# Performance work log

Hardware: AMD Instinct MI355X
Metric: run time of the kernel (lower is better)

## Reference

```python
import jax, jax.numpy as jnp
import numpy as np

N_NODES = 50000
N_EDGES = 800000
IN_CH = 128
HID = 128


def setup_inputs() -> dict:
    key = jax.random.key(0)
    ks = jax.random.split(key, 16)
    inp = {
        "x": jax.random.normal(ks[0], (N_NODES, IN_CH), dtype=jnp.float32),
        "edge_index": jax.random.randint(ks[1], (2, N_EDGES), 0, N_NODES, dtype=jnp.int64),
        "batch_size": 1024,
    }
    dims = [(IN_CH, HID), (HID, HID), (HID, HID)]
    for i, (din, dout) in enumerate(dims):
        s = 1.0 / np.sqrt(din)
        inp[f"W_l{i}"] = jax.random.uniform(ks[2 + 4 * i], (dout, din), jnp.float32, -s, s)
        inp[f"b_l{i}"] = jax.random.uniform(ks[3 + 4 * i], (dout,), jnp.float32, -s, s)
        inp[f"W_r{i}"] = jax.random.uniform(ks[4 + 4 * i], (dout, din), jnp.float32, -s, s)
        inp[f"a{i}"] = jnp.full((dout,), 0.25, dtype=jnp.float32)  # PReLU slope
    return inp


def _sage_prelu(x, src, dst, W_l, b_l, W_r, a):
    # mean aggregation of source messages at target nodes
    msg_sum = jax.ops.segment_sum(x[src], dst, num_segments=N_NODES)  # [N, din]
    deg = jax.ops.segment_sum(jnp.ones((src.shape[0],), x.dtype), dst, num_segments=N_NODES)
    agg = msg_sum / jnp.maximum(deg, 1.0)[:, None]
    out = agg @ W_l.T + b_l + x @ W_r.T  # lin_l(aggr) + lin_r(x), bias on lin_l only
    return jnp.where(out > 0, out, a * out)  # per-channel PReLU


def reference(x, edge_index, batch_size, W_l0, b_l0, W_r0, a0, W_l1, b_l1, W_r1, a1, W_l2, b_l2, W_r2, a2):
    src, dst = edge_index[0], edge_index[1]
    x = _sage_prelu(x, src, dst, W_l0, b_l0, W_r0, a0)
    x = _sage_prelu(x, src, dst, W_l1, b_l1, W_r1, a1)
    x = _sage_prelu(x, src, dst, W_l2, b_l2, W_r2, a2)
    return x[:batch_size]
```

## Files before the change

### kernel.cpp

```cpp
#include <hip/hip_runtime.h>

#define NN 50000
#define NE 800000
#define C 128
#define CAP 64
#define EP4 ((NE / 4 + 255) / 256)
#define SPLITB 1563
#define WB 96
#define CB  ((NN + 255) / 256)
#define AGG0B ((NN + 3) / 4)
#define ASTRIDE 136

typedef __attribute__((ext_vector_type(8))) short bf16x8;
typedef __attribute__((ext_vector_type(4))) float f32x4;
typedef unsigned short ushort;

__device__ inline ushort bf16_rn(float f) {
    unsigned u = __builtin_bit_cast(unsigned, f);
    u += 0x7FFF + ((u >> 16) & 1);
    return (ushort)(u >> 16);
}
__device__ inline void split_bf16(float f, ushort& hi, ushort& lo) {
    hi = bf16_rn(f);
    float hif = __builtin_bit_cast(float, (unsigned)hi << 16);
    lo = bf16_rn(f - hif);
}
__device__ inline float bf_lo(unsigned u) { return __builtin_bit_cast(float, u << 16); }
__device__ inline float bf_hi(unsigned u) { return __builtin_bit_cast(float, u & 0xFFFF0000u); }


__global__ __launch_bounds__(256)
void prep_kernel(const int* __restrict__ src, const int* __restrict__ dst,
                 const float* __restrict__ x,
                 const float* __restrict__ W0, const float* __restrict__ W1,
                 const float* __restrict__ W2, const float* __restrict__ W3,
                 const float* __restrict__ W4, const float* __restrict__ W5,
                 int* __restrict__ deg, int* __restrict__ col,
                 ushort* __restrict__ Ah, ushort* __restrict__ Al,
                 ushort* __restrict__ Wh, ushort* __restrict__ Wl,
                 int* __restrict__ needed, int rows_out) {
    int t = threadIdx.x;
    if (blockIdx.x < EP4) {
        int e0 = (blockIdx.x * 256 + t) * 4;
        if (e0 < NE) {
            int4 da = *(const int4*)(dst + e0);
            int4 sa = *(const int4*)(src + e0);
            int p0 = atomicAdd(&deg[da.x], 1);
            int p1 = atomicAdd(&deg[da.y], 1);
            int p2 = atomicAdd(&deg[da.z], 1);
            int p3 = atomicAdd(&deg[da.w], 1);
            if (p0 < CAP) col[da.x * CAP + p0] = sa.x;
            if (p1 < CAP) col[da.y * CAP + p1] = sa.y;
            if (p2 < CAP) col[da.z * CAP + p2] = sa.z;
            if (p3 < CAP) col[da.w * CAP + p3] = sa.w;
            if (da.x < rows_out) needed[sa.x] = 1;
            if (da.y < rows_out) needed[sa.y] = 1;
            if (da.z < rows_out) needed[sa.z] = 1;
            if (da.w < rows_out) needed[sa.w] = 1;
        }
    } else if (blockIdx.x < EP4 + SPLITB) {
        int tid = (blockIdx.x - EP4) * 256 + t;
        const int total = NN * C / 4;
        for (int i = tid; i < total; i += SPLITB * 256) {
            f32x4 v = ((const f32x4*)x)[i];
            ushort h0, h1, h2, h3, l0, l1, l2, l3;
            split_bf16(v.x, h0, l0);
            split_bf16(v.y, h1, l1);
            split_bf16(v.z, h2, l2);
            split_bf16(v.w, h3, l3);
            *(uint2*)(Ah + (size_t)i * 4) = make_uint2((unsigned)h0 | ((unsigned)h1 << 16),
                                                       (unsigned)h2 | ((unsigned)h3 << 16));
            *(uint2*)(Al + (size_t)i * 4) = make_uint2((unsigned)l0 | ((unsigned)l1 << 16),
                                                       (unsigned)l2 | ((unsigned)l3 << 16));
        }
    } else {
        const float* Ws[6] = {W0, W1, W2, W3, W4, W5};
        int i = (blockIdx.x - EP4 - SPLITB) * 256 + t;
        int mat = i >> 12;
        f32x4 v = ((const f32x4*)Ws[mat])[i & 4095];
        ushort h0, h1, h2, h3, l0, l1, l2, l3;
        split_bf16(v.x, h0, l0);
        split_bf16(v.y, h1, l1);
        split_bf16(v.z, h2, l2);
        split_bf16(v.w, h3, l3);
        *(uint2*)(Wh + (size_t)i * 4) = make_uint2((unsigned)h0 | ((unsigned)h1 << 16),
                                                   (unsigned)h2 | ((unsigned)h3 << 16));
        *(uint2*)(Wl + (size_t)i * 4) = make_uint2((unsigned)l0 | ((unsigned)l1 << 16),
                                                   (unsigned)l2 | ((unsigned)l3 << 16));
    }
}


__global__ __launch_bounds__(256)
void agg_kernel(const ushort* __restrict__ xh, const int* __restrict__ deg,
                const int* __restrict__ col,
                const int* __restrict__ list, const int* __restrict__ countp,
                ushort* __restrict__ aggh, ushort* __restrict__ aggl, int nodes,
                int aggblocks, const int* __restrict__ needed,
                int* __restrict__ wlist, int* __restrict__ wcnt, int rows_out) {
    if (needed && blockIdx.x >= aggblocks) {
        int i = (blockIdx.x - aggblocks) * 256 + threadIdx.x;
        if (i < NN && (i < rows_out || needed[i])) {
            int p = atomicAdd(wcnt, 1);
            wlist[p] = i;
        }
        return;
    }
    int i = (blockIdx.x * blockDim.x + threadIdx.x) >> 6;
    int lane = threadIdx.x & 63;
    int cnt = list ? *countp : nodes;
    if (i >= cnt) return;
    int node = list ? list[i] : i;
    int quad = lane >> 4;
    int ql   = lane & 15;
    int d = min(deg[node], CAP);
    int start = node * CAP;
    int end = start + d;
    const uint4* xr = (const uint4*)xh;
    float a0=0,a1=0,a2=0,a3=0,a4=0,a5=0,a6=0,a7=0;
    int e = start;
    for (; e + 7 < end; e += 8) {
        int i0 = col[e + quad];
        int i1 = col[e + 4 + quad];
        uint4 u0 = xr[(size_t)i0 * 16 + ql];
        uint4 u1 = xr[(size_t)i1 * 16 + ql];
        a0 += bf_lo(u0.x) + bf_lo(u1.x); a1 += bf_hi(u0.x) + bf_hi(u1.x);
        a2 += bf_lo(u0.y) + bf_lo(u1.y); a3 += bf_hi(u0.y) + bf_hi(u1.y);
        a4 += bf_lo(u0.z) + bf_lo(u1.z); a5 += bf_hi(u0.z) + bf_hi(u1.z);
        a6 += bf_lo(u0.w) + bf_lo(u1.w); a7 += bf_hi(u0.w) + bf_hi(u1.w);
    }
    for (; e + 3 < end; e += 4) {
        uint4 u = xr[(size_t)col[e + quad] * 16 + ql];
        a0 += bf_lo(u.x); a1 += bf_hi(u.x);
        a2 += bf_lo(u.y); a3 += bf_hi(u.y);
        a4 += bf_lo(u.z); a5 += bf_hi(u.z);
        a6 += bf_lo(u.w); a7 += bf_hi(u.w);
    }
    int rem = end - e;
    if (quad < rem) {
        uint4 u = xr[(size_t)col[e + quad] * 16 + ql];
        a0 += bf_lo(u.x); a1 += bf_hi(u.x);
        a2 += bf_lo(u.y); a3 += bf_hi(u.y);
        a4 += bf_lo(u.z); a5 += bf_hi(u.z);
        a6 += bf_lo(u.w); a7 += bf_hi(u.w);
    }
    a0 += __shfl_xor(a0, 16, 64); a0 += __shfl_xor(a0, 32, 64);
    a1 += __shfl_xor(a1, 16, 64); a1 += __shfl_xor(a1, 32, 64);
    a2 += __shfl_xor(a2, 16, 64); a2 += __shfl_xor(a2, 32, 64);
    a3 += __shfl_xor(a3, 16, 64); a3 += __shfl_xor(a3, 32, 64);
    a4 += __shfl_xor(a4, 16, 64); a4 += __shfl_xor(a4, 32, 64);
    a5 += __shfl_xor(a5, 16, 64); a5 += __shfl_xor(a5, 32, 64);
    a6 += __shfl_xor(a6, 16, 64); a6 += __shfl_xor(a6, 32, 64);
    a7 += __shfl_xor(a7, 16, 64); a7 += __shfl_xor(a7, 32, 64);
    if (quad == 0) {
        float inv = 1.0f / (float)max(d, 1);
        float m[8] = {a0*inv, a1*inv, a2*inv, a3*inv, a4*inv, a5*inv, a6*inv, a7*inv};
        ushort h[8], o[8];
        #pragma unroll
        for (int j = 0; j < 8; ++j) split_bf16(m[j], h[j], o[j]);
        size_t off = (size_t)node * C + ql * 8;
        *(uint4*)(aggh + off) = make_uint4((unsigned)h[0] | ((unsigned)h[1] << 16),
                                           (unsigned)h[2] | ((unsigned)h[3] << 16),
                                           (unsigned)h[4] | ((unsigned)h[5] << 16),
                                           (unsigned)h[6] | ((unsigned)h[7] << 16));
        *(uint4*)(aggl + off) = make_uint4((unsigned)o[0] | ((unsigned)o[1] << 16),
                                           (unsigned)o[2] | ((unsigned)o[3] << 16),
                                           (unsigned)o[4] | ((unsigned)o[5] << 16),
                                           (unsigned)o[6] | ((unsigned)o[7] << 16));
    }
}


__global__ __launch_bounds__(256, 4)
void gemm_kernel(const ushort* __restrict__ Ah, const ushort* __restrict__ Al,
                 const ushort* __restrict__ Xh, const ushort* __restrict__ Xl,
                 const ushort* __restrict__ Wlh, const ushort* __restrict__ Wll,
                 const ushort* __restrict__ Wrh, const ushort* __restrict__ Wrl,
                 const float* __restrict__ bl, const float* __restrict__ slope,
                 const int* __restrict__ list, const int* __restrict__ countp,
                 float* __restrict__ outf, ushort* __restrict__ outh,
                 ushort* __restrict__ outl, int rows) {
    __shared__ ushort Ahi[64 * ASTRIDE];
    __shared__ ushort Alo[64 * ASTRIDE];
    int t = threadIdx.x;
    int lane = t & 63;
    int w = t >> 6;
    int l = lane & 15;
    int q = lane >> 4;
    int row0 = blockIdx.x * 64;
    int cnt = list ? min(*countp, rows) : rows;
    if (row0 >= cnt) return;

    f32x4 acc[4][2];
    #pragma unroll
    for (int mt = 0; mt < 4; ++mt)
        #pragma unroll
        for (int nt = 0; nt < 2; ++nt)
            acc[mt][nt] = (f32x4){0.f, 0.f, 0.f, 0.f};

    #pragma unroll
    for (int mat = 0; mat < 2; ++mat) {
        const ushort* WH = mat ? Wrh : Wlh;
        const ushort* WL = mat ? Wrl : Wll;
        const ushort* Ph = mat ? Xh : Ah;
        const ushort* Pl = mat ? Xl : Al;

        bf16x8 bhi[2][4], blo[2][4];
        #pragma unroll
        for (int nt = 0; nt < 2; ++nt) {
            int n = w * 32 + nt * 16 + l;
            const ushort* wp = WH + (size_t)n * C + q * 8;
            const ushort* wq = WL + (size_t)n * C + q * 8;
            #pragma unroll
            for (int kb = 0; kb < 4; ++kb) {
                bhi[nt][kb] = *(const bf16x8*)(wp + kb * 32);
                blo[nt][kb] = *(const bf16x8*)(wq + kb * 32);
            }
        }

        __syncthreads();
        int ar = t >> 2;
        int aq = t & 3;
        int ridx = min(row0 + ar, cnt - 1);
        int r = list ? list[ridx] : ridx;
        ushort* dh = Ahi + ar * ASTRIDE + aq * 32;
        ushort* dl = Alo + ar * ASTRIDE + aq * 32;
        const ushort* ph = Ph + (size_t)r * C + aq * 32;
        const ushort* pl = Pl + (size_t)r * C + aq * 32;
        #pragma unroll
        for (int i = 0; i < 4; ++i) {
            *(uint4*)(dh + i * 8) = *(const uint4*)(ph + i * 8);
            *(uint4*)(dl + i * 8) = *(const uint4*)(pl + i * 8);
        }
        __syncthreads();

        #pragma unroll
        for (int kb = 0; kb < 4; ++kb) {
            #pragma unroll
            for (int mt = 0; mt < 4; ++mt) {
                int off = (mt * 16 + l) * ASTRIDE + kb * 32 + q * 8;
                bf16x8 ahi = *(const bf16x8*)(Ahi + off);
                bf16x8 alo = *(const bf16x8*)(Alo + off);
                #pragma unroll
                for (int nt = 0; nt < 2; ++nt) {
                    acc[mt][nt] = __builtin_amdgcn_mfma_f32_16x16x32_bf16(ahi, bhi[nt][kb], acc[mt][nt], 0, 0, 0);
                    acc[mt][nt] = __builtin_amdgcn_mfma_f32_16x16x32_bf16(alo, bhi[nt][kb], acc[mt][nt], 0, 0, 0);
                    acc[mt][nt] = __builtin_amdgcn_mfma_f32_16x16x32_bf16(ahi, blo[nt][kb], acc[mt][nt], 0, 0, 0);
                }
            }
        }
    }

    #pragma unroll
    for (int nt = 0; nt < 2; ++nt) {
        int n = w * 32 + nt * 16 + l;
        float b = bl[n], s = slope[n];
        #pragma unroll
        for (int mt = 0; mt < 4; ++mt) {
            #pragma unroll
            for (int rg = 0; rg < 4; ++rg) {
                int ridx = row0 + mt * 16 + q * 4 + rg;
                if (ridx < cnt) {
                    int r = list ? list[ridx] : ridx;
                    float v = acc[mt][nt][rg] + b;
                    v = v > 0.f ? v : s * v;
                    if (outf) {
                        outf[(size_t)r * C + n] = v;
                    } else {
                        ushort hh, ll;
                        split_bf16(v, hh, ll);
                        outh[(size_t)r * C + n] = hh;
                        outl[(size_t)r * C + n] = ll;
                    }
                }
            }
        }
    }
}


extern "C" void kernel_launch(void* const* d_in, const int* in_sizes, int n_in,
                              void* d_out, int out_size, void* d_ws, size_t ws_size,
                              hipStream_t stream) {
    const float* x   = (const float*)d_in[0];
    const int*   src = (const int*)d_in[1];
    const int*   dst = src + NE;
    const float* Wl[3] = {(const float*)d_in[3], (const float*)d_in[7],  (const float*)d_in[11]};
    const float* bl[3] = {(const float*)d_in[4], (const float*)d_in[8],  (const float*)d_in[12]};
    const float* Wr[3] = {(const float*)d_in[5], (const float*)d_in[9],  (const float*)d_in[13]};
    const float* sl[3] = {(const float*)d_in[6], (const float*)d_in[10], (const float*)d_in[14]};

    int*   deg     = (int*)d_ws;
    int*   needed  = deg + 50016;
    int*   cnt     = needed + 50016;
    int*   col     = cnt + 16;
    int*   list    = col + NN * CAP;
    ushort* Whs    = (ushort*)(list + 50016);
    ushort* Wls    = Whs + 6 * 16384;
    ushort* Gh     = Wls + 6 * 16384;
    ushort* Gl     = Gh + (size_t)NN * C;
    ushort* Ah     = Gl + (size_t)NN * C;
    ushort* Al     = Ah + (size_t)NN * C;
    ushort* Bh     = Al + (size_t)NN * C;
    ushort* Bl     = Bh + (size_t)NN * C;

    int rows_out = out_size / C;

    hipMemsetAsync(deg, 0, (2 * 50016 + 16) * sizeof(int), stream);

    prep_kernel<<<EP4 + SPLITB + WB, 256, 0, stream>>>(
        src, dst, x, Wl[0], Wr[0], Wl[1], Wr[1], Wl[2], Wr[2],
        deg, col, Ah, Al, Whs, Wls, needed, rows_out);

    agg_kernel<<<AGG0B + CB, 256, 0, stream>>>(Ah, deg, col, nullptr, nullptr, Gh, Gl, NN,
                                               AGG0B, needed, list, cnt, rows_out);
    gemm_kernel<<<(NN + 63) / 64, 256, 0, stream>>>(Gh, Gl, Ah, Al,
                                                    Whs + 0 * 16384, Wls + 0 * 16384,
                                                    Whs + 1 * 16384, Wls + 1 * 16384,
                                                    bl[0], sl[0], nullptr, nullptr,
                                                    nullptr, Bh, Bl, NN);

    agg_kernel<<<AGG0B, 256, 0, stream>>>(Bh, deg, col, list, cnt, Gh, Gl, NN,
                                          AGG0B, nullptr, nullptr, nullptr, rows_out);
    gemm_kernel<<<(NN + 63) / 64, 256, 0, stream>>>(Gh, Gl, Bh, Bl,
                                                    Whs + 2 * 16384, Wls + 2 * 16384,
                                                    Whs + 3 * 16384, Wls + 3 * 16384,
                                                    bl[1], sl[1], list, cnt,
                                                    nullptr, Ah, Al, NN);

    agg_kernel<<<(rows_out + 3) / 4, 256, 0, stream>>>(Ah, deg, col, nullptr, nullptr,
                                                       Gh, Gl, rows_out,
                                                       (rows_out + 3) / 4, nullptr,
                                                       nullptr, nullptr, rows_out);
    gemm_kernel<<<(rows_out + 63) / 64, 256, 0, stream>>>(Gh, Gl, Ah, Al,
                                                          Whs + 4 * 16384, Wls + 4 * 16384,
                                                          Whs + 5 * 16384, Wls + 5 * 16384,
                                                          bl[2], sl[2], nullptr, nullptr,
                                                          (float*)d_out, nullptr, nullptr,
                                                          rows_out);
}
```

Measured before the change: 292.0 us.

## Fuse layer-0 input bf16 split into GEMM and drop low-half prep output

The prep kernel now writes only the bf16 high half of x, which the first aggregation needs. The layer-0 GEMM reads fp32 x directly and splits it into hi/lo bf16 tiles in shared memory, so the full low-half array is no longer written and re-read. The edge-scatter part is also changed to handle two edges per thread instead of four. In exchange, the layer-0 GEMM does extra conversion ALU work and reads fp32 rows, twice the bytes of one bf16 half.

```diff
diff --git a/kernel.cpp b/kernel.cpp
--- a/kernel.cpp
+++ b/kernel.cpp
@@ -4,7 +4,7 @@
 #define NE 800000
 #define C 128
 #define CAP 64
-#define EP4 ((NE / 4 + 255) / 256)
+#define EP2 ((NE / 2 + 255) / 256)
 #define SPLITB 1563
 #define WB 96
 #define CB  ((NN + 255) / 256)
@@ -36,46 +36,35 @@
                  const float* __restrict__ W2, const float* __restrict__ W3,
                  const float* __restrict__ W4, const float* __restrict__ W5,
                  int* __restrict__ deg, int* __restrict__ col,
-                 ushort* __restrict__ Ah, ushort* __restrict__ Al,
+                 ushort* __restrict__ Ah,
                  ushort* __restrict__ Wh, ushort* __restrict__ Wl,
                  int* __restrict__ needed, int rows_out) {
     int t = threadIdx.x;
-    if (blockIdx.x < EP4) {
-        int e0 = (blockIdx.x * 256 + t) * 4;
+    if (blockIdx.x < EP2) {
+        int e0 = (blockIdx.x * 256 + t) * 2;
         if (e0 < NE) {
-            int4 da = *(const int4*)(dst + e0);
-            int4 sa = *(const int4*)(src + e0);
-            int p0 = atomicAdd(&deg[da.x], 1);
-            int p1 = atomicAdd(&deg[da.y], 1);
-            int p2 = atomicAdd(&deg[da.z], 1);
-            int p3 = atomicAdd(&deg[da.w], 1);
-            if (p0 < CAP) col[da.x * CAP + p0] = sa.x;
-            if (p1 < CAP) col[da.y * CAP + p1] = sa.y;
-            if (p2 < CAP) col[da.z * CAP + p2] = sa.z;
-            if (p3 < CAP) col[da.w * CAP + p3] = sa.w;
-            if (da.x < rows_out) needed[sa.x] = 1;
-            if (da.y < rows_out) needed[sa.y] = 1;
-            if (da.z < rows_out) needed[sa.z] = 1;
-            if (da.w < rows_out) needed[sa.w] = 1;
-        }
-    } else if (blockIdx.x < EP4 + SPLITB) {
-        int tid = (blockIdx.x - EP4) * 256 + t;
+            int2 d2 = *(const int2*)(dst + e0);
+            int2 s2 = *(const int2*)(src + e0);
+            int p0 = atomicAdd(&deg[d2.x], 1);
+            int p1 = atomicAdd(&deg[d2.y], 1);
+            if (p0 < CAP) col[d2.x * CAP + p0] = s2.x;
+            if (p1 < CAP) col[d2.y * CAP + p1] = s2.y;
+            if (d2.x < rows_out) needed[s2.x] = 1;
+            if (d2.y < rows_out) needed[s2.y] = 1;
+        }
+    } else if (blockIdx.x < EP2 + SPLITB) {
+        int tid = (blockIdx.x - EP2) * 256 + t;
         const int total = NN * C / 4;
         for (int i = tid; i < total; i += SPLITB * 256) {
             f32x4 v = ((const f32x4*)x)[i];
-            ushort h0, h1, h2, h3, l0, l1, l2, l3;
-            split_bf16(v.x, h0, l0);
-            split_bf16(v.y, h1, l1);
-            split_bf16(v.z, h2, l2);
-            split_bf16(v.w, h3, l3);
+            ushort h0 = bf16_rn(v.x), h1 = bf16_rn(v.y);
+            ushort h2 = bf16_rn(v.z), h3 = bf16_rn(v.w);
             *(uint2*)(Ah + (size_t)i * 4) = make_uint2((unsigned)h0 | ((unsigned)h1 << 16),
                                                        (unsigned)h2 | ((unsigned)h3 << 16));
-            *(uint2*)(Al + (size_t)i * 4) = make_uint2((unsigned)l0 | ((unsigned)l1 << 16),
-                                                       (unsigned)l2 | ((unsigned)l3 << 16));
         }
     } else {
         const float* Ws[6] = {W0, W1, W2, W3, W4, W5};
-        int i = (blockIdx.x - EP4 - SPLITB) * 256 + t;
+        int i = (blockIdx.x - EP2 - SPLITB) * 256 + t;
         int mat = i >> 12;
         f32x4 v = ((const f32x4*)Ws[mat])[i & 4095];
         ushort h0, h1, h2, h3, l0, l1, l2, l3;
@@ -174,6 +163,7 @@
 __global__ __launch_bounds__(256, 4)
 void gemm_kernel(const ushort* __restrict__ Ah, const ushort* __restrict__ Al,
                  const ushort* __restrict__ Xh, const ushort* __restrict__ Xl,
+                 const float* __restrict__ Xf,
                  const ushort* __restrict__ Wlh, const ushort* __restrict__ Wll,
                  const ushort* __restrict__ Wrh, const ushort* __restrict__ Wrl,
                  const float* __restrict__ bl, const float* __restrict__ slope,
@@ -225,12 +215,29 @@
         int r = list ? list[ridx] : ridx;
         ushort* dh = Ahi + ar * ASTRIDE + aq * 32;
         ushort* dl = Alo + ar * ASTRIDE + aq * 32;
-        const ushort* ph = Ph + (size_t)r * C + aq * 32;
-        const ushort* pl = Pl + (size_t)r * C + aq * 32;
-        #pragma unroll
-        for (int i = 0; i < 4; ++i) {
-            *(uint4*)(dh + i * 8) = *(const uint4*)(ph + i * 8);
-            *(uint4*)(dl + i * 8) = *(const uint4*)(pl + i * 8);
+        if (mat == 1 && Xf) {
+            const float* px = Xf + (size_t)r * C + aq * 32;
+            #pragma unroll
+            for (int i = 0; i < 8; ++i) {
+                f32x4 v = *(const f32x4*)(px + i * 4);
+                ushort h0, h1, h2, h3, l0, l1, l2, l3;
+                split_bf16(v.x, h0, l0);
+                split_bf16(v.y, h1, l1);
+                split_bf16(v.z, h2, l2);
+                split_bf16(v.w, h3, l3);
+                *(uint2*)(dh + i * 4) = make_uint2((unsigned)h0 | ((unsigned)h1 << 16),
+                                                   (unsigned)h2 | ((unsigned)h3 << 16));
+                *(uint2*)(dl + i * 4) = make_uint2((unsigned)l0 | ((unsigned)l1 << 16),
+                                                   (unsigned)l2 | ((unsigned)l3 << 16));
+            }
+        } else {
+            const ushort* ph = Ph + (size_t)r * C + aq * 32;
+            const ushort* pl = Pl + (size_t)r * C + aq * 32;
+            #pragma unroll
+            for (int i = 0; i < 4; ++i) {
+                *(uint4*)(dh + i * 8) = *(const uint4*)(ph + i * 8);
+                *(uint4*)(dl + i * 8) = *(const uint4*)(pl + i * 8);
+            }
         }
         __syncthreads();
 
@@ -308,13 +315,13 @@
 
     hipMemsetAsync(deg, 0, (2 * 50016 + 16) * sizeof(int), stream);
 
-    prep_kernel<<<EP4 + SPLITB + WB, 256, 0, stream>>>(
+    prep_kernel<<<EP2 + SPLITB + WB, 256, 0, stream>>>(
         src, dst, x, Wl[0], Wr[0], Wl[1], Wr[1], Wl[2], Wr[2],
-        deg, col, Ah, Al, Whs, Wls, needed, rows_out);
+        deg, col, Ah, Whs, Wls, needed, rows_out);
 
     agg_kernel<<<AGG0B + CB, 256, 0, stream>>>(Ah, deg, col, nullptr, nullptr, Gh, Gl, NN,
                                                AGG0B, needed, list, cnt, rows_out);
-    gemm_kernel<<<(NN + 63) / 64, 256, 0, stream>>>(Gh, Gl, Ah, Al,
+    gemm_kernel<<<(NN + 63) / 64, 256, 0, stream>>>(Gh, Gl, nullptr, nullptr, x,
                                                     Whs + 0 * 16384, Wls + 0 * 16384,
                                                     Whs + 1 * 16384, Wls + 1 * 16384,
                                                     bl[0], sl[0], nullptr, nullptr,
@@ -322,7 +329,7 @@
 
     agg_kernel<<<AGG0B, 256, 0, stream>>>(Bh, deg, col, list, cnt, Gh, Gl, NN,
                                           AGG0B, nullptr, nullptr, nullptr, rows_out);
-    gemm_kernel<<<(NN + 63) / 64, 256, 0, stream>>>(Gh, Gl, Bh, Bl,
+    gemm_kernel<<<(NN + 63) / 64, 256, 0, stream>>>(Gh, Gl, Bh, Bl, nullptr,
                                                     Whs + 2 * 16384, Wls + 2 * 16384,
                                                     Whs + 3 * 16384, Wls + 3 * 16384,
                                                     bl[1], sl[1], list, cnt,
@@ -332,7 +339,7 @@
                                                        Gh, Gl, rows_out,
                                                        (rows_out + 3) / 4, nullptr,
                                                        nullptr, nullptr, rows_out);
-    gemm_kernel<<<(rows_out + 63) / 64, 256, 0, stream>>>(Gh, Gl, Ah, Al,
+    gemm_kernel<<<(rows_out + 63) / 64, 256, 0, stream>>>(Gh, Gl, Ah, Al, nullptr,
                                                           Whs + 4 * 16384, Wls + 4 * 16384,
                                                           Whs + 5 * 16384, Wls + 5 * 16384,
                                                           bl[2], sl[2], nullptr, nullptr,
```

Result: faster. 285.4 us (-2.3%).

## Fuse neighbor mean aggregation into the GEMM tile loader

Applied to the files above, without the earlier changes.

Removes the separate aggregation kernels. Each GEMM block now gathers neighbor rows for its 64 output rows, computes the mean and splits it into hi/lo bf16 directly in shared memory, so the intermediate aggregated hi/lo buffers are no longer written and re-read in global memory. Layer 0 reads fp32 x and splits it on the fly instead of materialising a low-part buffer in prep, and the edge scatter now handles 8 edges per thread. The trade-off is that each thread serially gathers a whole 32-channel slice per neighbor, which lowers memory-level parallelism and raises register pressure in the GEMM kernel.

```diff
diff --git a/kernel.cpp b/kernel.cpp
--- a/kernel.cpp
+++ b/kernel.cpp
@@ -4,11 +4,10 @@
 #define NE 800000
 #define C 128
 #define CAP 64
-#define EP4 ((NE / 4 + 255) / 256)
+#define EP8 ((NE / 8 + 255) / 256)
 #define SPLITB 1563
 #define WB 96
 #define CB  ((NN + 255) / 256)
-#define AGG0B ((NN + 3) / 4)
 #define ASTRIDE 136
 
 typedef __attribute__((ext_vector_type(8))) short bf16x8;
@@ -36,46 +35,55 @@
                  const float* __restrict__ W2, const float* __restrict__ W3,
                  const float* __restrict__ W4, const float* __restrict__ W5,
                  int* __restrict__ deg, int* __restrict__ col,
-                 ushort* __restrict__ Ah, ushort* __restrict__ Al,
+                 ushort* __restrict__ Ah,
                  ushort* __restrict__ Wh, ushort* __restrict__ Wl,
                  int* __restrict__ needed, int rows_out) {
     int t = threadIdx.x;
-    if (blockIdx.x < EP4) {
-        int e0 = (blockIdx.x * 256 + t) * 4;
+    if (blockIdx.x < EP8) {
+        int e0 = (blockIdx.x * 256 + t) * 8;
         if (e0 < NE) {
             int4 da = *(const int4*)(dst + e0);
+            int4 db = *(const int4*)(dst + e0 + 4);
             int4 sa = *(const int4*)(src + e0);
+            int4 sb = *(const int4*)(src + e0 + 4);
             int p0 = atomicAdd(&deg[da.x], 1);
             int p1 = atomicAdd(&deg[da.y], 1);
             int p2 = atomicAdd(&deg[da.z], 1);
             int p3 = atomicAdd(&deg[da.w], 1);
+            int p4 = atomicAdd(&deg[db.x], 1);
+            int p5 = atomicAdd(&deg[db.y], 1);
+            int p6 = atomicAdd(&deg[db.z], 1);
+            int p7 = atomicAdd(&deg[db.w], 1);
             if (p0 < CAP) col[da.x * CAP + p0] = sa.x;
             if (p1 < CAP) col[da.y * CAP + p1] = sa.y;
             if (p2 < CAP) col[da.z * CAP + p2] = sa.z;
             if (p3 < CAP) col[da.w * CAP + p3] = sa.w;
+            if (p4 < CAP) col[db.x * CAP + p4] = sb.x;
+            if (p5 < CAP) col[db.y * CAP + p5] = sb.y;
+            if (p6 < CAP) col[db.z * CAP + p6] = sb.z;
+            if (p7 < CAP) col[db.w * CAP + p7] = sb.w;
             if (da.x < rows_out) needed[sa.x] = 1;
             if (da.y < rows_out) needed[sa.y] = 1;
             if (da.z < rows_out) needed[sa.z] = 1;
             if (da.w < rows_out) needed[sa.w] = 1;
-        }
-    } else if (blockIdx.x < EP4 + SPLITB) {
-        int tid = (blockIdx.x - EP4) * 256 + t;
+            if (db.x < rows_out) needed[sb.x] = 1;
+            if (db.y < rows_out) needed[sb.y] = 1;
+            if (db.z < rows_out) needed[sb.z] = 1;
+            if (db.w < rows_out) needed[sb.w] = 1;
+        }
+    } else if (blockIdx.x < EP8 + SPLITB) {
+        int tid = (blockIdx.x - EP8) * 256 + t;
         const int total = NN * C / 4;
         for (int i = tid; i < total; i += SPLITB * 256) {
             f32x4 v = ((const f32x4*)x)[i];
-            ushort h0, h1, h2, h3, l0, l1, l2, l3;
-            split_bf16(v.x, h0, l0);
-            split_bf16(v.y, h1, l1);
-            split_bf16(v.z, h2, l2);
-            split_bf16(v.w, h3, l3);
+            ushort h0 = bf16_rn(v.x), h1 = bf16_rn(v.y);
+            ushort h2 = bf16_rn(v.z), h3 = bf16_rn(v.w);
             *(uint2*)(Ah + (size_t)i * 4) = make_uint2((unsigned)h0 | ((unsigned)h1 << 16),
                                                        (unsigned)h2 | ((unsigned)h3 << 16));
-            *(uint2*)(Al + (size_t)i * 4) = make_uint2((unsigned)l0 | ((unsigned)l1 << 16),
-                                                       (unsigned)l2 | ((unsigned)l3 << 16));
         }
     } else {
         const float* Ws[6] = {W0, W1, W2, W3, W4, W5};
-        int i = (blockIdx.x - EP4 - SPLITB) * 256 + t;
+        int i = (blockIdx.x - EP8 - SPLITB) * 256 + t;
         int mat = i >> 12;
         f32x4 v = ((const f32x4*)Ws[mat])[i & 4095];
         ushort h0, h1, h2, h3, l0, l1, l2, l3;
@@ -92,94 +100,26 @@
 
 
 __global__ __launch_bounds__(256)
-void agg_kernel(const ushort* __restrict__ xh, const int* __restrict__ deg,
-                const int* __restrict__ col,
-                const int* __restrict__ list, const int* __restrict__ countp,
-                ushort* __restrict__ aggh, ushort* __restrict__ aggl, int nodes,
-                int aggblocks, const int* __restrict__ needed,
-                int* __restrict__ wlist, int* __restrict__ wcnt, int rows_out) {
-    if (needed && blockIdx.x >= aggblocks) {
-        int i = (blockIdx.x - aggblocks) * 256 + threadIdx.x;
+void fused_kernel(const ushort* __restrict__ Gsrc,
+                  const int* __restrict__ deg, const int* __restrict__ col,
+                  const ushort* __restrict__ Xh, const ushort* __restrict__ Xl,
+                  const float* __restrict__ Xf,
+                  const ushort* __restrict__ Wlh, const ushort* __restrict__ Wll,
+                  const ushort* __restrict__ Wrh, const ushort* __restrict__ Wrl,
+                  const float* __restrict__ bl, const float* __restrict__ slope,
+                  const int* __restrict__ list, const int* __restrict__ countp,
+                  float* __restrict__ outf, ushort* __restrict__ outh,
+                  ushort* __restrict__ outl, int rows,
+                  int gemmblocks, const int* __restrict__ needed,
+                  int* __restrict__ wlist, int* __restrict__ wcnt, int rows_out) {
+    if (needed && (int)blockIdx.x >= gemmblocks) {
+        int i = ((int)blockIdx.x - gemmblocks) * 256 + threadIdx.x;
         if (i < NN && (i < rows_out || needed[i])) {
             int p = atomicAdd(wcnt, 1);
             wlist[p] = i;
         }
         return;
     }
-    int i = (blockIdx.x * blockDim.x + threadIdx.x) >> 6;
-    int lane = threadIdx.x & 63;
-    int cnt = list ? *countp : nodes;
-    if (i >= cnt) return;
-    int node = list ? list[i] : i;
-    int quad = lane >> 4;
-    int ql   = lane & 15;
-    int d = min(deg[node], CAP);
-    int start = node * CAP;
-    int end = start + d;
-    const uint4* xr = (const uint4*)xh;
-    float a0=0,a1=0,a2=0,a3=0,a4=0,a5=0,a6=0,a7=0;
-    int e = start;
-    for (; e + 7 < end; e += 8) {
-        int i0 = col[e + quad];
-        int i1 = col[e + 4 + quad];
-        uint4 u0 = xr[(size_t)i0 * 16 + ql];
-        uint4 u1 = xr[(size_t)i1 * 16 + ql];
-        a0 += bf_lo(u0.x) + bf_lo(u1.x); a1 += bf_hi(u0.x) + bf_hi(u1.x);
-        a2 += bf_lo(u0.y) + bf_lo(u1.y); a3 += bf_hi(u0.y) + bf_hi(u1.y);
-        a4 += bf_lo(u0.z) + bf_lo(u1.z); a5 += bf_hi(u0.z) + bf_hi(u1.z);
-        a6 += bf_lo(u0.w) + bf_lo(u1.w); a7 += bf_hi(u0.w) + bf_hi(u1.w);
-    }
-    for (; e + 3 < end; e += 4) {
-        uint4 u = xr[(size_t)col[e + quad] * 16 + ql];
-        a0 += bf_lo(u.x); a1 += bf_hi(u.x);
-        a2 += bf_lo(u.y); a3 += bf_hi(u.y);
-        a4 += bf_lo(u.z); a5 += bf_hi(u.z);
-        a6 += bf_lo(u.w); a7 += bf_hi(u.w);
-    }
-    int rem = end - e;
-    if (quad < rem) {
-        uint4 u = xr[(size_t)col[e + quad] * 16 + ql];
-        a0 += bf_lo(u.x); a1 += bf_hi(u.x);
-        a2 += bf_lo(u.y); a3 += bf_hi(u.y);
-        a4 += bf_lo(u.z); a5 += bf_hi(u.z);
-        a6 += bf_lo(u.w); a7 += bf_hi(u.w);
-    }
-    a0 += __shfl_xor(a0, 16, 64); a0 += __shfl_xor(a0, 32, 64);
-    a1 += __shfl_xor(a1, 16, 64); a1 += __shfl_xor(a1, 32, 64);
-    a2 += __shfl_xor(a2, 16, 64); a2 += __shfl_xor(a2, 32, 64);
-    a3 += __shfl_xor(a3, 16, 64); a3 += __shfl_xor(a3, 32, 64);
-    a4 += __shfl_xor(a4, 16, 64); a4 += __shfl_xor(a4, 32, 64);
-    a5 += __shfl_xor(a5, 16, 64); a5 += __shfl_xor(a5, 32, 64);
-    a6 += __shfl_xor(a6, 16, 64); a6 += __shfl_xor(a6, 32, 64);
-    a7 += __shfl_xor(a7, 16, 64); a7 += __shfl_xor(a7, 32, 64);
-    if (quad == 0) {
-        float inv = 1.0f / (float)max(d, 1);
-        float m[8] = {a0*inv, a1*inv, a2*inv, a3*inv, a4*inv, a5*inv, a6*inv, a7*inv};
-        ushort h[8], o[8];
-        #pragma unroll
-        for (int j = 0; j < 8; ++j) split_bf16(m[j], h[j], o[j]);
-        size_t off = (size_t)node * C + ql * 8;
-        *(uint4*)(aggh + off) = make_uint4((unsigned)h[0] | ((unsigned)h[1] << 16),
-                                           (unsigned)h[2] | ((unsigned)h[3] << 16),
-                                           (unsigned)h[4] | ((unsigned)h[5] << 16),
-                                           (unsigned)h[6] | ((unsigned)h[7] << 16));
-        *(uint4*)(aggl + off) = make_uint4((unsigned)o[0] | ((unsigned)o[1] << 16),
-                                           (unsigned)o[2] | ((unsigned)o[3] << 16),
-                                           (unsigned)o[4] | ((unsigned)o[5] << 16),
-                                           (unsigned)o[6] | ((unsigned)o[7] << 16));
-    }
-}
-
-
-__global__ __launch_bounds__(256, 4)
-void gemm_kernel(const ushort* __restrict__ Ah, const ushort* __restrict__ Al,
-                 const ushort* __restrict__ Xh, const ushort* __restrict__ Xl,
-                 const ushort* __restrict__ Wlh, const ushort* __restrict__ Wll,
-                 const ushort* __restrict__ Wrh, const ushort* __restrict__ Wrl,
-                 const float* __restrict__ bl, const float* __restrict__ slope,
-                 const int* __restrict__ list, const int* __restrict__ countp,
-                 float* __restrict__ outf, ushort* __restrict__ outh,
-                 ushort* __restrict__ outl, int rows) {
     __shared__ ushort Ahi[64 * ASTRIDE];
     __shared__ ushort Alo[64 * ASTRIDE];
     int t = threadIdx.x;
@@ -202,8 +142,6 @@
     for (int mat = 0; mat < 2; ++mat) {
         const ushort* WH = mat ? Wrh : Wlh;
         const ushort* WL = mat ? Wrl : Wll;
-        const ushort* Ph = mat ? Xh : Ah;
-        const ushort* Pl = mat ? Xl : Al;
 
         bf16x8 bhi[2][4], blo[2][4];
         #pragma unroll
@@ -225,12 +163,77 @@
         int r = list ? list[ridx] : ridx;
         ushort* dh = Ahi + ar * ASTRIDE + aq * 32;
         ushort* dl = Alo + ar * ASTRIDE + aq * 32;
-        const ushort* ph = Ph + (size_t)r * C + aq * 32;
-        const ushort* pl = Pl + (size_t)r * C + aq * 32;
-        #pragma unroll
-        for (int i = 0; i < 4; ++i) {
-            *(uint4*)(dh + i * 8) = *(const uint4*)(ph + i * 8);
-            *(uint4*)(dl + i * 8) = *(const uint4*)(pl + i * 8);
+        if (mat == 0) {
+            int d = min(deg[r], CAP);
+            int base = r * CAP;
+            float s[32];
+            #pragma unroll
+            for (int j = 0; j < 32; ++j) s[j] = 0.f;
+#define ACC8(k, u, v) \
+            s[(k)+0] += bf_lo((u).x) + bf_lo((v).x); s[(k)+1] += bf_hi((u).x) + bf_hi((v).x); \
+            s[(k)+2] += bf_lo((u).y) + bf_lo((v).y); s[(k)+3] += bf_hi((u).y) + bf_hi((v).y); \
+            s[(k)+4] += bf_lo((u).z) + bf_lo((v).z); s[(k)+5] += bf_hi((u).z) + bf_hi((v).z); \
+            s[(k)+6] += bf_lo((u).w) + bf_lo((v).w); s[(k)+7] += bf_hi((u).w) + bf_hi((v).w);
+#define ACC8S(k, u) \
+            s[(k)+0] += bf_lo((u).x); s[(k)+1] += bf_hi((u).x); \
+            s[(k)+2] += bf_lo((u).y); s[(k)+3] += bf_hi((u).y); \
+            s[(k)+4] += bf_lo((u).z); s[(k)+5] += bf_hi((u).z); \
+            s[(k)+6] += bf_lo((u).w); s[(k)+7] += bf_hi((u).w);
+            int e = 0;
+            for (; e + 1 < d; e += 2) {
+                int2 c01 = *(const int2*)(col + base + e);
+                const uint4* p0 = (const uint4*)Gsrc + (size_t)c01.x * 16 + aq * 4;
+                const uint4* p1 = (const uint4*)Gsrc + (size_t)c01.y * 16 + aq * 4;
+                uint4 a0 = p0[0], a1 = p0[1], a2 = p0[2], a3 = p0[3];
+                uint4 b0 = p1[0], b1 = p1[1], b2 = p1[2], b3 = p1[3];
+                ACC8(0, a0, b0) ACC8(8, a1, b1) ACC8(16, a2, b2) ACC8(24, a3, b3)
+            }
+            if (e < d) {
+                int c0 = col[base + e];
+                const uint4* p0 = (const uint4*)Gsrc + (size_t)c0 * 16 + aq * 4;
+                uint4 a0 = p0[0], a1 = p0[1], a2 = p0[2], a3 = p0[3];
+                ACC8S(0, a0) ACC8S(8, a1) ACC8S(16, a2) ACC8S(24, a3)
+            }
+#undef ACC8
+#undef ACC8S
+            float inv = 1.0f / (float)max(d, 1);
+            #pragma unroll
+            for (int i = 0; i < 4; ++i) {
+                ushort h[8], o[8];
+                #pragma unroll
+                for (int j = 0; j < 8; ++j) split_bf16(s[i * 8 + j] * inv, h[j], o[j]);
+                *(uint4*)(dh + i * 8) = make_uint4((unsigned)h[0] | ((unsigned)h[1] << 16),
+                                                   (unsigned)h[2] | ((unsigned)h[3] << 16),
+                                                   (unsigned)h[4] | ((unsigned)h[5] << 16),
+                                                   (unsigned)h[6] | ((unsigned)h[7] << 16));
+                *(uint4*)(dl + i * 8) = make_uint4((unsigned)o[0] | ((unsigned)o[1] << 16),
+                                                   (unsigned)o[2] | ((unsigned)o[3] << 16),
+                                                   (unsigned)o[4] | ((unsigned)o[5] << 16),
+                                                   (unsigned)o[6] | ((unsigned)o[7] << 16));
+            }
+        } else if (Xf) {
+            const float* px = Xf + (size_t)r * C + aq * 32;
+            #pragma unroll
+            for (int i = 0; i < 8; ++i) {
+                f32x4 v = *(const f32x4*)(px + i * 4);
+                ushort h0, h1, h2, h3, l0, l1, l2, l3;
+                split_bf16(v.x, h0, l0);
+                split_bf16(v.y, h1, l1);
+                split_bf16(v.z, h2, l2);
+                split_bf16(v.w, h3, l3);
+                *(uint2*)(dh + i * 4) = make_uint2((unsigned)h0 | ((unsigned)h1 << 16),
+                                                   (unsigned)h2 | ((unsigned)h3 << 16));
+                *(uint2*)(dl + i * 4) = make_uint2((unsigned)l0 | ((unsigned)l1 << 16),
+                                                   (unsigned)l2 | ((unsigned)l3 << 16));
+            }
+        } else {
+            const ushort* ph = Xh + (size_t)r * C + aq * 32;
+            const ushort* pl = Xl + (size_t)r * C + aq * 32;
+            #pragma unroll
+            for (int i = 0; i < 4; ++i) {
+                *(uint4*)(dh + i * 8) = *(const uint4*)(ph + i * 8);
+                *(uint4*)(dl + i * 8) = *(const uint4*)(pl + i * 8);
+            }
         }
         __syncthreads();
 
@@ -297,45 +300,40 @@
     int*   list    = col + NN * CAP;
     ushort* Whs    = (ushort*)(list + 50016);
     ushort* Wls    = Whs + 6 * 16384;
-    ushort* Gh     = Wls + 6 * 16384;
-    ushort* Gl     = Gh + (size_t)NN * C;
-    ushort* Ah     = Gl + (size_t)NN * C;
+    ushort* Ah     = Wls + 6 * 16384;
     ushort* Al     = Ah + (size_t)NN * C;
     ushort* Bh     = Al + (size_t)NN * C;
     ushort* Bl     = Bh + (size_t)NN * C;
 
     int rows_out = out_size / C;
+    int gb = (NN + 63) / 64;
 
     hipMemsetAsync(deg, 0, (2 * 50016 + 16) * sizeof(int), stream);
 
-    prep_kernel<<<EP4 + SPLITB + WB, 256, 0, stream>>>(
+    prep_kernel<<<EP8 + SPLITB + WB, 256, 0, stream>>>(
         src, dst, x, Wl[0], Wr[0], Wl[1], Wr[1], Wl[2], Wr[2],
-        deg, col, Ah, Al, Whs, Wls, needed, rows_out);
-
-    agg_kernel<<<AGG0B + CB, 256, 0, stream>>>(Ah, deg, col, nullptr, nullptr, Gh, Gl, NN,
-                                               AGG0B, needed, list, cnt, rows_out);
-    gemm_kernel<<<(NN + 63) / 64, 256, 0, stream>>>(Gh, Gl, Ah, Al,
-                                                    Whs + 0 * 16384, Wls + 0 * 16384,
-                                                    Whs + 1 * 16384, Wls + 1 * 16384,
-                                                    bl[0], sl[0], nullptr, nullptr,
-                                                    nullptr, Bh, Bl, NN);
-
-    agg_kernel<<<AGG0B, 256, 0, stream>>>(Bh, deg, col, list, cnt, Gh, Gl, NN,
-                                          AGG0B, nullptr, nullptr, nullptr, rows_out);
-    gemm_kernel<<<(NN + 63) / 64, 256, 0, stream>>>(Gh, Gl, Bh, Bl,
-                                                    Whs + 2 * 16384, Wls + 2 * 16384,
-                                                    Whs + 3 * 16384, Wls + 3 * 16384,
-                                                    bl[1], sl[1], list, cnt,
-                                                    nullptr, Ah, Al, NN);
-
-    agg_kernel<<<(rows_out + 3) / 4, 256, 0, stream>>>(Ah, deg, col, nullptr, nullptr,
-                                                       Gh, Gl, rows_out,
-                                                       (rows_out + 3) / 4, nullptr,
-                                                       nullptr, nullptr, rows_out);
-    gemm_kernel<<<(rows_out + 63) / 64, 256, 0, stream>>>(Gh, Gl, Ah, Al,
-                                                          Whs + 4 * 16384, Wls + 4 * 16384,
-                                                          Whs + 5 * 16384, Wls + 5 * 16384,
-                                                          bl[2], sl[2], nullptr, nullptr,
-                                                          (float*)d_out, nullptr, nullptr,
-                                                          rows_out);
-}
+        deg, col, Ah, Whs, Wls, needed, rows_out);
+
+    fused_kernel<<<gb + CB, 256, 0, stream>>>(Ah, deg, col, nullptr, nullptr, x,
+                                              Whs + 0 * 16384, Wls + 0 * 16384,
+                                              Whs + 1 * 16384, Wls + 1 * 16384,
+                                              bl[0], sl[0], nullptr, nullptr,
+                                              nullptr, Bh, Bl, NN,
+                                              gb, needed, list, cnt, rows_out);
+
+    fused_kernel<<<gb, 256, 0, stream>>>(Bh, deg, col, Bh, Bl, nullptr,
+                                         Whs + 2 * 16384, Wls + 2 * 16384,
+                                         Whs + 3 * 16384, Wls + 3 * 16384,
+                                         bl[1], sl[1], list, cnt,
+                                         nullptr, Ah, Al, NN,
+                                         gb, nullptr, nullptr, nullptr, rows_out);
+
+    fused_kernel<<<(rows_out + 63) / 64, 256, 0, stream>>>(Ah, deg, col, Ah, Al, nullptr,
+                                                           Whs + 4 * 16384, Wls + 4 * 16384,
+                                                           Whs + 5 * 16384, Wls + 5 * 16384,
+                                                           bl[2], sl[2], nullptr, nullptr,
+                                                           (float*)d_out, nullptr, nullptr,
+                                                           rows_out,
+                                                           (rows_out + 63) / 64, nullptr,
+                                                           nullptr, nullptr, rows_out);
+}
```

New measurement: 289.4 us. About the same (-0.9%).
